# Optimization experiments

Measured on AMD Instinct MI355X. Metric: run time of the kernel, lower is better.

## Reference

```python
import jax, jax.numpy as jnp
import numpy as np

B, E, CIN, COUT, K, H, W = 32, 5, 256, 256, 3, 56, 56
R = 4
SCALING = 16.0 / R  # lora_alpha / r


def setup_inputs() -> dict:
    key = jax.random.key(0)
    k1, k2, k3, k4, k5 = jax.random.split(key, 5)
    x = jax.random.normal(k1, (B, CIN, H, W), dtype=jnp.float32)
    scores = jax.random.normal(k2, (B, E), dtype=jnp.float32)
    weight = jax.random.normal(k3, (COUT, CIN, K, K), dtype=jnp.float32) * 0.02
    lora_A = jax.random.normal(k4, (E, R * K, CIN * K), dtype=jnp.float32) * 0.02
    lora_B = jax.random.normal(k5, (E, COUT * K, R * K), dtype=jnp.float32) * 0.02
    return {"x": x, "scores": scores, "weight": weight, "lora_A": lora_A, "lora_B": lora_B}


def reference(x, scores, weight, lora_A, lora_B):
    b = x.shape[0]
    # hard top-1 expert one-hot with straight-through estimator (GetMask backward: d scores = d one_hot)
    hard = jax.nn.one_hot(jnp.argmax(scores, axis=1), scores.shape[1], dtype=scores.dtype)  # [B,E]
    one_hot = scores + jax.lax.stop_gradient(hard - scores)
    # per-expert LoRA delta weights: [E, O*K, I*K] -> [E, O, I, K, K]
    delta = jnp.einsum('eor,eri->eoi', lora_B, lora_A)
    delta = delta.reshape(delta.shape[0], *weight.shape) * SCALING
    # per-sample aggregated weights: [B, O, I, K, K]
    agg = weight[None] + jnp.einsum('be,eoikl->boikl', one_hot, delta)
    # grouped conv2d with groups = batch
    out = jax.lax.conv_general_dilated(
        x.reshape(1, -1, x.shape[2], x.shape[3]),          # [1, B*Cin, H, W]
        agg.reshape(-1, *agg.shape[-3:]),                   # [B*O, Cin, K, K]
        window_strides=(1, 1),
        padding=((1, 1), (1, 1)),
        feature_group_count=b,
        dimension_numbers=('NCHW', 'OIHW', 'NCHW'),
    )
    return out.reshape(b, -1, out.shape[2], out.shape[3])
```

## Files before the change

kernel.cpp:

```cpp
#include <hip/hip_runtime.h>
#include <hip/hip_bf16.h>

#define BB    32
#define EE    5
#define HH    56
#define WW    56
#define KKC   2304
#define SCAL  4.0f

typedef __attribute__((ext_vector_type(8))) short short8;
typedef __attribute__((ext_vector_type(4))) float f32x4;

#define WF2_PER_E  (9 * 8 * 256 * 32)
#define XP2_PER_BC (58 * 58 * 32)

#define NXPB (58 * BB)
#define NPRB (256 * EE)

__device__ __forceinline__ void gload_lds16(const void* g, void* l) {
    __builtin_amdgcn_global_load_lds(
        (const __attribute__((address_space(1))) unsigned int*)g,
        (__attribute__((address_space(3))) unsigned int*)l, 16, 0, 0);
}

__device__ __forceinline__ unsigned short f2bf(float f) {
    unsigned int u = __float_as_uint(f);
    return (unsigned short)((u + 0x7FFFu + ((u >> 16) & 1u)) >> 16);
}

__global__ __launch_bounds__(256) void lora_prep_xpose_kernel(
    const float* __restrict__ x,
    const float* __restrict__ weight,
    const float* __restrict__ lora_A,
    const float* __restrict__ lora_B,
    unsigned short* __restrict__ Wf2,
    unsigned short* __restrict__ xpad2)
{
    const int tid = threadIdx.x;

    if (blockIdx.x >= NXPB) {
        const int pid = blockIdx.x - NXPB;
        const int co  = pid & 255;
        const int e   = pid >> 8;
        const int ci  = tid;

        float Bsv[3][12];
        #pragma unroll
        for (int q = 0; q < 3; ++q)
            #pragma unroll
            for (int r = 0; r < 12; ++r)
                Bsv[q][r] = lora_B[((size_t)e * 768 + co * 3 + q) * 12 + r];

        const float* As   = lora_A + (size_t)e * 12 * 768;
        const float* wrow = weight + (size_t)co * KKC + ci * 9;
        const int cic = ci >> 5, ci32 = ci & 31;
        #pragma unroll
        for (int tap = 0; tap < 9; ++tap) {
            int idx  = ci * 9 + tap;
            int q    = idx / 768;
            int i768 = idx - q * 768;
            float acc = 0.f;
            #pragma unroll
            for (int r = 0; r < 12; ++r)
                acc += Bsv[q][r] * As[r * 768 + i768];
            float v = wrow[tap] + SCAL * acc;
            Wf2[((size_t)((e * 9 + tap) * 8 + cic)) * 8192 + co * 32 + ci32] = f2bf(v);
        }
        return;
    }

    const int bid = blockIdx.x;
    const int b   = bid / 58;
    const int rp  = bid - b * 58;
    unsigned short* xp = xpad2 + (size_t)b * 8 * XP2_PER_BC;
    const uint4 z4 = {0u, 0u, 0u, 0u};

    if (rp == 0 || rp == 57) {
        for (int t = tid; t < 1856; t += 256) {
            int cic = t / 232, q = t % 232;
            ((uint4*)(xp + ((size_t)cic * 3364 + rp * 58) * 32))[q] = z4;
        }
        return;
    }
    if (tid < 64) {
        int cic = tid >> 3, which = (tid >> 2) & 1, q = tid & 3;
        ((uint4*)(xp + ((size_t)cic * 3364 + rp * 58 + (which ? 57 : 0)) * 32))[q] = z4;
    }

    const int row = rp - 1;
    const float* xb = x + (size_t)b * 256 * 3136 + row * 56;

    float v[7][8];
    #pragma unroll
    for (int s = 0; s < 7; ++s) {
        int gid   = s * 256 + tid;
        int cic   = gid / 224;
        int rem   = gid - cic * 224;
        int c     = rem >> 2;
        int gphys = rem & 3;
        int gq    = gphys ^ (((c + 1) >> 1) & 3);
        const float* src = xb + (size_t)(cic * 32 + gq * 8) * 3136 + c;
        #pragma unroll
        for (int k = 0; k < 8; ++k)
            v[s][k] = src[(size_t)k * 3136];
    }

    unsigned short* xrow = xp + ((size_t)rp * 58 + 1) * 32;
    #pragma unroll
    for (int s = 0; s < 7; ++s) {
        int gid = s * 256 + tid;
        int cic = gid / 224;
        int rem = gid - cic * 224;
        unsigned int wv[4];
        #pragma unroll
        for (int j = 0; j < 4; ++j) {
            unsigned short lo = f2bf(v[s][2 * j + 0]);
            unsigned short hi = f2bf(v[s][2 * j + 1]);
            wv[j] = (unsigned int)lo | ((unsigned int)hi << 16);
        }
        uint4 pk; pk.x = wv[0]; pk.y = wv[1]; pk.z = wv[2]; pk.w = wv[3];
        *(uint4*)(xrow + (size_t)cic * 107648 + (size_t)rem * 8) = pk;
    }
}

__global__ __launch_bounds__(256, 2) void lora_conv_mfma_kernel(
    const unsigned short* __restrict__ xpad2,
    const unsigned short* __restrict__ Wf2,
    const float* __restrict__ scores,
    float* __restrict__ out)
{
    const int y0   = blockIdx.x * 4;
    const int co0  = blockIdx.y * 128;
    const int b    = blockIdx.z;
    const int tid  = threadIdx.x;
    const int wave = tid >> 6;
    const int lane = tid & 63;
    const int ln15 = lane & 15;
    const int quad = lane >> 4;
    const int wm2  = (wave & 1) * 64;
    const int wn2  = (wave >> 1) * 112;

    __shared__ short8 Xlds[2][1392];
    __shared__ int sExp;

    if (tid == 0) {
        const float* s = scores + b * EE;
        int best = 0; float bv = s[0];
        #pragma unroll
        for (int j = 1; j < EE; ++j) { float v = s[j]; if (v > bv) { bv = v; best = j; } }
        sExp = best;
    }

    const unsigned short* xsrc0 = xpad2 + (size_t)b * 8 * XP2_PER_BC + y0 * 58 * 32;

    auto stage = [&](int cic, int buf) {
        const unsigned short* src = xsrc0 + (size_t)cic * XP2_PER_BC;
        char* dst = (char*)&Xlds[buf][0];
        #pragma unroll
        for (int i = 0; i < 5; ++i) {
            int G = i * 256 + tid;
            gload_lds16(src + (size_t)G * 8, dst + (size_t)G * 16);
        }
        if (tid < 112) {
            int G = 1280 + tid;
            gload_lds16(src + (size_t)G * 8, dst + (size_t)G * 16);
        }
    };

    stage(0, 0);
    __syncthreads();
    const int e = sExp;

    const unsigned short* Wb =
        Wf2 + (size_t)e * WF2_PER_E + (co0 + wm2 + ln15) * 32 + quad * 8;

    int pg01[7], pg2[7];
    #pragma unroll
    for (int tn = 0; tn < 7; ++tn) {
        int pos = wn2 + tn * 16 + ln15;
        int r = pos / 56, c = pos - r * 56;
        int o[3];
        #pragma unroll
        for (int k2 = 0; k2 < 3; ++k2) {
            int cc = c + k2;
            int g  = quad ^ ((cc >> 1) & 3);
            o[k2] = (r * 232 + cc * 4 + g) * 16;
        }
        pg01[tn] = o[0] | (o[1] << 16);
        pg2[tn]  = o[2];
    }

    f32x4 acc[4][7];
    #pragma unroll
    for (int tm = 0; tm < 4; ++tm)
        #pragma unroll
        for (int tn = 0; tn < 7; ++tn)
            acc[tm][tn] = (f32x4){0.f, 0.f, 0.f, 0.f};

    short8 A0[4], A1[4], A2[4];
    #pragma unroll
    for (int tm = 0; tm < 4; ++tm) {
        A0[tm] = *(const short8*)(Wb + 0 * 65536 + tm * 512);
        A1[tm] = *(const short8*)(Wb + 1 * 65536 + tm * 512);
    }

    for (int cic = 0; cic < 8; ++cic) {
        const unsigned short* Wc = Wb + cic * 8192;
        const char* Xb = (const char*)&Xlds[cic & 1][0];
        #pragma unroll
        for (int tap = 0; tap < 9; ++tap) {
            if (tap == 0 && cic < 7) stage(cic + 1, (cic & 1) ^ 1);
            if (tap < 7) {
                #pragma unroll
                for (int tm = 0; tm < 4; ++tm)
                    A2[tm] = *(const short8*)(Wc + (tap + 2) * 65536 + tm * 512);
            } else if (cic < 7) {
                #pragma unroll
                for (int tm = 0; tm < 4; ++tm)
                    A2[tm] = *(const short8*)(Wc + 8192 + (tap - 7) * 65536 + tm * 512);
            }
            const int k1 = tap / 3, k2 = tap % 3;
            __builtin_amdgcn_s_setprio(1);
            #pragma unroll
            for (int tn = 0; tn < 7; ++tn) {
                int off = (k2 == 0) ? (pg01[tn] & 0xffff)
                        : (k2 == 1) ? (pg01[tn] >> 16)
                                    : pg2[tn];
                short8 bfr = *(const short8*)(Xb + off + k1 * 3712);
                #pragma unroll
                for (int tm = 0; tm < 4; ++tm)
                    acc[tm][tn] = __builtin_amdgcn_mfma_f32_16x16x32_bf16(
                        A0[tm], bfr, acc[tm][tn], 0, 0, 0);
            }
            __builtin_amdgcn_s_setprio(0);
            #pragma unroll
            for (int tm = 0; tm < 4; ++tm) { A0[tm] = A1[tm]; A1[tm] = A2[tm]; }
        }
        if (cic < 7) __syncthreads();
    }

    #pragma unroll
    for (int tm = 0; tm < 4; ++tm) {
        #pragma unroll
        for (int tn = 0; tn < 7; ++tn) {
            int n = wn2 + tn * 16 + ln15;
            int r = n / 56, c = n - r * 56;
            #pragma unroll
            for (int reg = 0; reg < 4; ++reg) {
                int m = co0 + wm2 + tm * 16 + quad * 4 + reg;
                out[(((size_t)b * 256 + m) * HH + y0 + r) * WW + c] = acc[tm][tn][reg];
            }
        }
    }
}

extern "C" void kernel_launch(void* const* d_in, const int* in_sizes, int n_in,
                              void* d_out, int out_size, void* d_ws, size_t ws_size,
                              hipStream_t stream) {
    const float* x      = (const float*)d_in[0];
    const float* scores = (const float*)d_in[1];
    const float* weight = (const float*)d_in[2];
    const float* lora_A = (const float*)d_in[3];
    const float* lora_B = (const float*)d_in[4];
    float* out = (float*)d_out;

    char* ws = (char*)d_ws;
    unsigned short* Wf2   = (unsigned short*)(ws + 256);
    unsigned short* xpad2 = (unsigned short*)(ws + 256 + (size_t)EE * WF2_PER_E * 2);

    lora_prep_xpose_kernel<<<dim3(NXPB + NPRB), 256, 0, stream>>>(
        x, weight, lora_A, lora_B, Wf2, xpad2);
    lora_conv_mfma_kernel<<<dim3(14, 2, BB), 256, 0, stream>>>(xpad2, Wf2, scores, out);
}
```

Baseline: 354.3 us.

## Stage lora_A and x rows through LDS in the prep kernel

```diff
diff --git a/kernel.cpp b/kernel.cpp
--- a/kernel.cpp
+++ b/kernel.cpp
@@ -36,10 +36,14 @@
     unsigned short* __restrict__ Wf2,
     unsigned short* __restrict__ xpad2)
 {
+    __shared__ union ShU {
+        float As[12 * 768];
+        float xs[8][32][56];
+    } sh;
     const int tid = threadIdx.x;
 
-    if (blockIdx.x >= NXPB) {
-        const int pid = blockIdx.x - NXPB;
+    if (blockIdx.x < NPRB) {
+        const int pid = blockIdx.x;
         const int co  = pid & 255;
         const int e   = pid >> 8;
         const int ci  = tid;
@@ -51,7 +55,10 @@
             for (int r = 0; r < 12; ++r)
                 Bsv[q][r] = lora_B[((size_t)e * 768 + co * 3 + q) * 12 + r];
 
-        const float* As   = lora_A + (size_t)e * 12 * 768;
+        for (int i = tid; i < 12 * 768; i += 256)
+            sh.As[i] = lora_A[e * 12 * 768 + i];
+        __syncthreads();
+
         const float* wrow = weight + (size_t)co * KKC + ci * 9;
         const int cic = ci >> 5, ci32 = ci & 31;
         #pragma unroll
@@ -62,14 +69,14 @@
             float acc = 0.f;
             #pragma unroll
             for (int r = 0; r < 12; ++r)
-                acc += Bsv[q][r] * As[r * 768 + i768];
+                acc += Bsv[q][r] * sh.As[r * 768 + i768];
             float v = wrow[tap] + SCAL * acc;
             Wf2[((size_t)((e * 9 + tap) * 8 + cic)) * 8192 + co * 32 + ci32] = f2bf(v);
         }
         return;
     }
 
-    const int bid = blockIdx.x;
+    const int bid = blockIdx.x - NPRB;
     const int b   = bid / 58;
     const int rp  = bid - b * 58;
     unsigned short* xp = xpad2 + (size_t)b * 8 * XP2_PER_BC;
@@ -90,20 +97,15 @@
     const int row = rp - 1;
     const float* xb = x + (size_t)b * 256 * 3136 + row * 56;
 
-    float v[7][8];
-    #pragma unroll
-    for (int s = 0; s < 7; ++s) {
-        int gid   = s * 256 + tid;
-        int cic   = gid / 224;
-        int rem   = gid - cic * 224;
-        int c     = rem >> 2;
-        int gphys = rem & 3;
-        int gq    = gphys ^ (((c + 1) >> 1) & 3);
-        const float* src = xb + (size_t)(cic * 32 + gq * 8) * 3136 + c;
-        #pragma unroll
-        for (int k = 0; k < 8; ++k)
-            v[s][k] = src[(size_t)k * 3136];
-    }
+    char* lds0 = (char*)&sh.xs[0][0][0];
+    #pragma unroll
+    for (int i = 0; i < 14; ++i) {
+        int g  = i * 256 + tid;
+        int ch = g / 14;
+        int c4 = g - ch * 14;
+        gload_lds16(xb + (size_t)ch * 3136 + c4 * 4, lds0 + (size_t)g * 16);
+    }
+    __syncthreads();
 
     unsigned short* xrow = xp + ((size_t)rp * 58 + 1) * 32;
     #pragma unroll
@@ -111,11 +113,14 @@
         int gid = s * 256 + tid;
         int cic = gid / 224;
         int rem = gid - cic * 224;
+        int c   = rem >> 2;
+        int gphys = rem & 3;
+        int gq  = gphys ^ (((c + 1) >> 1) & 3);
         unsigned int wv[4];
         #pragma unroll
         for (int j = 0; j < 4; ++j) {
-            unsigned short lo = f2bf(v[s][2 * j + 0]);
-            unsigned short hi = f2bf(v[s][2 * j + 1]);
+            unsigned short lo = f2bf(sh.xs[cic][gq * 8 + 2 * j + 0][c]);
+            unsigned short hi = f2bf(sh.xs[cic][gq * 8 + 2 * j + 1][c]);
             wv[j] = (unsigned int)lo | ((unsigned int)hi << 16);
         }
         uint4 pk; pk.x = wv[0]; pk.y = wv[1]; pk.z = wv[2]; pk.w = wv[3];
@@ -268,7 +273,7 @@
     unsigned short* Wf2   = (unsigned short*)(ws + 256);
     unsigned short* xpad2 = (unsigned short*)(ws + 256 + (size_t)EE * WF2_PER_E * 2);
 
-    lora_prep_xpose_kernel<<<dim3(NXPB + NPRB), 256, 0, stream>>>(
+    lora_prep_xpose_kernel<<<dim3(NPRB + NXPB), 256, 0, stream>>>(
         x, weight, lora_A, lora_B, Wf2, xpad2);
     lora_conv_mfma_kernel<<<dim3(14, 2, BB), 256, 0, stream>>>(xpad2, Wf2, scores, out);
 }
```

New measurement: 318.9 us. 10.0% less time.
